# Kernel optimization log

Hardware: AMD Instinct MI355X
Metric: run time of the kernel (lower is better)

Reference implementation:

```python
import jax, jax.numpy as jnp
import numpy as np

ALPHA = 1.0
BETA = 0.5

B, N, E = 4096, 4096, 16384


def setup_inputs() -> dict:
    key = jax.random.key(0)
    k1, k2, k3, k4, k5 = jax.random.split(key, 5)
    outputs = jax.random.normal(k1, (B, N), dtype=jnp.float32)
    targets = jax.random.uniform(k2, (B, N), dtype=jnp.float32)
    # per-node level weight (equivalent to node_levels dict -> level_weights lookup)
    level_w = jax.random.uniform(k3, (N,), dtype=jnp.float32)
    edge_src = jax.random.randint(k4, (E,), 0, N, dtype=jnp.int32)  # parent i
    edge_dst = jax.random.randint(k5, (E,), 0, N, dtype=jnp.int32)  # child  j
    return {"outputs": outputs, "targets": targets, "level_w": level_w,
            "edge_src": edge_src, "edge_dst": edge_dst}


def reference(outputs, targets, level_w, edge_src, edge_dst):
    # BCEWithLogits, reduction='none': softplus(x) - x*t (numerically stable)
    bce = jax.nn.softplus(outputs) - outputs * targets          # [B, N]
    weighted_bce = bce * level_w[None, :]                        # [B, N]

    probs = jax.nn.sigmoid(outputs)                              # [B, N]
    # for each edge (i=parent, j=child): consistency[:, j] += relu(p[:, j] - p[:, i])
    diff = jax.nn.relu(probs[:, edge_dst] - probs[:, edge_src])  # [B, E]
    consistency = jnp.zeros_like(probs).at[:, edge_dst].add(diff)  # [B, N]

    return ALPHA * weighted_bce.mean() + BETA * consistency.mean()
```

## Files before the change

kernel.cpp:

```cpp
#include <hip/hip_runtime.h>
#include <math.h>


#define ALPHA_C 1.0f
#define BETA_C  0.5f

constexpr int B = 4096;
constexpr int N = 4096;
constexpr int E = 16384;
constexpr int THREADS = 256;

__global__ __launch_bounds__(64) void init_out_kernel(float* out) {
    if (threadIdx.x == 0) out[0] = 0.0f;
}

__device__ __forceinline__ void fast_sig_sp(float x, float& p, float& sp) {
    float q = __expf(-fabsf(x));
    float d = 1.0f + q;
    float r = __builtin_amdgcn_rcpf(d);
    p  = (x >= 0.0f) ? r : q * r;
    sp = fmaxf(x, 0.0f) + __logf(d);
}

__global__ __launch_bounds__(THREADS) void hier_loss_row_kernel(
    const float* __restrict__ outputs,
    const float* __restrict__ targets,
    const float* __restrict__ level_w,
    const int*   __restrict__ edge_src,
    const int*   __restrict__ edge_dst,
    float*       __restrict__ out)
{
    __shared__ float p_lds[N];
    __shared__ float red[8];

    const int b   = blockIdx.x;
    const int tid = threadIdx.x;

    const float4* out4 = (const float4*)(outputs + (size_t)b * N);
    const float4* tgt4 = (const float4*)(targets + (size_t)b * N);
    const float4* lw4  = (const float4*)level_w;

    float s1 = 0.0f;
#pragma unroll
    for (int ii = 0; ii < N / 4 / THREADS; ++ii) {
        int i = tid + ii * THREADS;
        float4 x = out4[i];
        float4 t = tgt4[i];
        float4 w = lw4[i];
        float xs[4] = {x.x, x.y, x.z, x.w};
        float ts[4] = {t.x, t.y, t.z, t.w};
        float wv[4] = {w.x, w.y, w.z, w.w};
        float ps[4];
#pragma unroll
        for (int k = 0; k < 4; ++k) {
            float p, sp;
            fast_sig_sp(xs[k], p, sp);
            s1 = fmaf(wv[k], sp - xs[k] * ts[k], s1);
            ps[k] = p;
        }
        ((float4*)p_lds)[i] = make_float4(ps[0], ps[1], ps[2], ps[3]);
    }
    __syncthreads();

    float s2 = 0.0f;
    const int4* es4 = (const int4*)edge_src;
    const int4* ed4 = (const int4*)edge_dst;
#pragma unroll 4
    for (int i = tid; i < E / 4; i += THREADS) {
        int4 s = es4[i];
        int4 d = ed4[i];
        s2 += fmaxf(p_lds[d.x] - p_lds[s.x], 0.0f);
        s2 += fmaxf(p_lds[d.y] - p_lds[s.y], 0.0f);
        s2 += fmaxf(p_lds[d.z] - p_lds[s.z], 0.0f);
        s2 += fmaxf(p_lds[d.w] - p_lds[s.w], 0.0f);
    }

#pragma unroll
    for (int off = 32; off > 0; off >>= 1) {
        s1 += __shfl_down(s1, off, 64);
        s2 += __shfl_down(s2, off, 64);
    }
    const int wave = tid >> 6;
    const int lane = tid & 63;
    if (lane == 0) { red[wave] = s1; red[wave + 4] = s2; }
    __syncthreads();
    if (tid == 0) {
        float a = red[0] + red[1] + red[2] + red[3];
        float c = red[4] + red[5] + red[6] + red[7];
        const float inv = 1.0f / ((float)B * (float)N);
        atomicAdd(out, (ALPHA_C * a + BETA_C * c) * inv);
    }
}

extern "C" void kernel_launch(void* const* d_in, const int* in_sizes, int n_in,
                              void* d_out, int out_size, void* d_ws, size_t ws_size,
                              hipStream_t stream) {
    const float* outputs = (const float*)d_in[0];
    const float* targets = (const float*)d_in[1];
    const float* level_w = (const float*)d_in[2];
    const int*   edge_src = (const int*)d_in[3];
    const int*   edge_dst = (const int*)d_in[4];
    float* out = (float*)d_out;

    init_out_kernel<<<1, 64, 0, stream>>>(out);
    hier_loss_row_kernel<<<B, THREADS, 0, stream>>>(outputs, targets, level_w,
                                                    edge_src, edge_dst, out);
}
```

Measured before the change: 179.6 us.

## Process four batch rows per block with interleaved float4 LDS probabilities

Each block now handles four batch rows and stores their sigmoid probabilities interleaved as float4 per node in LDS. A single pair of edge-index loads and two 16-byte LDS reads then serve four rows' edge terms, cutting edge-index global traffic and LDS instruction count by four. Block size goes to 512 threads with 64KB LDS, and the reduction scratch reuses the probability buffer behind an extra barrier. The risks are lower occupancy from the larger LDS footprint and scalar rather than vectorized global loads for outputs and targets.

```diff
diff --git a/kernel.cpp b/kernel.cpp
--- a/kernel.cpp
+++ b/kernel.cpp
@@ -8,7 +8,8 @@
 constexpr int B = 4096;
 constexpr int N = 4096;
 constexpr int E = 16384;
-constexpr int THREADS = 256;
+constexpr int THREADS = 512;
+constexpr int R = 4;
 
 __global__ __launch_bounds__(64) void init_out_kernel(float* out) {
     if (threadIdx.x == 0) out[0] = 0.0f;
@@ -22,7 +23,14 @@
     sp = fmaxf(x, 0.0f) + __logf(d);
 }
 
-__global__ __launch_bounds__(THREADS) void hier_loss_row_kernel(
+__device__ __forceinline__ float edge4(const float4* __restrict__ p, int s, int d) {
+    float4 a = p[s];
+    float4 c = p[d];
+    return fmaxf(c.x - a.x, 0.0f) + fmaxf(c.y - a.y, 0.0f) +
+           fmaxf(c.z - a.z, 0.0f) + fmaxf(c.w - a.w, 0.0f);
+}
+
+__global__ __launch_bounds__(THREADS) void hier_loss_kernel(
     const float* __restrict__ outputs,
     const float* __restrict__ targets,
     const float* __restrict__ level_w,
@@ -30,49 +38,42 @@
     const int*   __restrict__ edge_dst,
     float*       __restrict__ out)
 {
-    __shared__ float p_lds[N];
-    __shared__ float red[8];
+    __shared__ float4 p_lds[N];
 
-    const int b   = blockIdx.x;
+    const int r0  = blockIdx.x * R;
     const int tid = threadIdx.x;
-
-    const float4* out4 = (const float4*)(outputs + (size_t)b * N);
-    const float4* tgt4 = (const float4*)(targets + (size_t)b * N);
-    const float4* lw4  = (const float4*)level_w;
 
     float s1 = 0.0f;
 #pragma unroll
-    for (int ii = 0; ii < N / 4 / THREADS; ++ii) {
-        int i = tid + ii * THREADS;
-        float4 x = out4[i];
-        float4 t = tgt4[i];
-        float4 w = lw4[i];
-        float xs[4] = {x.x, x.y, x.z, x.w};
-        float ts[4] = {t.x, t.y, t.z, t.w};
-        float wv[4] = {w.x, w.y, w.z, w.w};
-        float ps[4];
+    for (int j = 0; j < N / THREADS; ++j) {
+        const int n = tid + j * THREADS;
+        const float w = level_w[n];
+        float pv[R];
 #pragma unroll
-        for (int k = 0; k < 4; ++k) {
+        for (int r = 0; r < R; ++r) {
+            const float x = outputs[(size_t)(r0 + r) * N + n];
+            const float t = targets[(size_t)(r0 + r) * N + n];
             float p, sp;
-            fast_sig_sp(xs[k], p, sp);
-            s1 = fmaf(wv[k], sp - xs[k] * ts[k], s1);
-            ps[k] = p;
+            fast_sig_sp(x, p, sp);
+            s1 = fmaf(w, sp - x * t, s1);
+            pv[r] = p;
         }
-        ((float4*)p_lds)[i] = make_float4(ps[0], ps[1], ps[2], ps[3]);
+        p_lds[n] = make_float4(pv[0], pv[1], pv[2], pv[3]);
     }
     __syncthreads();
 
     float s2 = 0.0f;
     const int4* es4 = (const int4*)edge_src;
     const int4* ed4 = (const int4*)edge_dst;
-#pragma unroll 4
-    for (int i = tid; i < E / 4; i += THREADS) {
-        int4 s = es4[i];
-        int4 d = ed4[i];
-        s2 += fmaxf(p_lds[d.x] - p_lds[s.x], 0.0f);
-        s2 += fmaxf(p_lds[d.y] - p_lds[s.y], 0.0f);
-        s2 += fmaxf(p_lds[d.z] - p_lds[s.z], 0.0f);
-        s2 += fmaxf(p_lds[d.w] - p_lds[s.w], 0.0f);
+#pragma unroll
+    for (int j = 0; j < E / 4 / THREADS; ++j) {
+        const int i = tid + j * THREADS;
+        const int4 s = es4[i];
+        const int4 d = ed4[i];
+        s2 += edge4(p_lds, s.x, d.x);
+        s2 += edge4(p_lds, s.y, d.y);
+        s2 += edge4(p_lds, s.z, d.z);
+        s2 += edge4(p_lds, s.w, d.w);
     }
 
 #pragma unroll
@@ -80,13 +81,16 @@
         s1 += __shfl_down(s1, off, 64);
         s2 += __shfl_down(s2, off, 64);
     }
+    __syncthreads();
+    float* red = (float*)p_lds;
     const int wave = tid >> 6;
     const int lane = tid & 63;
-    if (lane == 0) { red[wave] = s1; red[wave + 4] = s2; }
+    if (lane == 0) { red[wave] = s1; red[8 + wave] = s2; }
     __syncthreads();
     if (tid == 0) {
-        float a = red[0] + red[1] + red[2] + red[3];
-        float c = red[4] + red[5] + red[6] + red[7];
+        float a = 0.0f, c = 0.0f;
+#pragma unroll
+        for (int w = 0; w < 8; ++w) { a += red[w]; c += red[8 + w]; }
         const float inv = 1.0f / ((float)B * (float)N);
         atomicAdd(out, (ALPHA_C * a + BETA_C * c) * inv);
     }
@@ -103,6 +107,6 @@
     float* out = (float*)d_out;
 
     init_out_kernel<<<1, 64, 0, stream>>>(out);
-    hier_loss_row_kernel<<<B, THREADS, 0, stream>>>(outputs, targets, level_w,
+    hier_loss_kernel<<<B / R, THREADS, 0, stream>>>(outputs, targets, level_w,
                                                     edge_src, edge_dst, out);
 }
```

After: 162.5 us. 9.5% less time.
